# Optimization experiments

Hardware: AMD Instinct MI355X
Metric: run time of the kernel (lower is better)

Reference implementation:

```python
import jax, jax.numpy as jnp
from jax import lax
import numpy as np

B = 8; T = 64000
NFFT = 1024; HOP = 256
SC = 20; KS = 1024; PAD = 512
HEADS = 8; GH = 64; GO = 32
SPEC_DIM = 32 * (NFFT // 4) // 2   # 4096
NODE_DIM = SC + SPEC_DIM           # 4116
EPS = 1e-5
NEG_SLOPE = 0.2


def setup_inputs() -> dict:
    ks = jax.random.split(jax.random.key(0), 12)
    f32 = jnp.float32
    def rn(k, shp, s):
        return jax.random.normal(k, shp, dtype=f32) * s
    return {
        "x": jax.random.normal(ks[0], (B, 1, T), dtype=f32),
        "sinc_w": rn(ks[1], (SC, 1, KS), 0.03),
        "conv1_w": rn(ks[2], (32, 1, 3, 3), 0.1),
        "conv1_b": jnp.zeros((32,), f32),
        "bn1_g": jnp.ones((32,), f32),
        "bn1_b": jnp.zeros((32,), f32),
        "conv2_w": rn(ks[3], (32, 32, 3, 3), 0.06),
        "conv2_b": jnp.zeros((32,), f32),
        "bn2_g": jnp.ones((32,), f32),
        "bn2_b": jnp.zeros((32,), f32),
        "gat1_W": rn(ks[4], (NODE_DIM, HEADS * GH), 0.015),
        "gat1_asrc": rn(ks[5], (HEADS, GH), 0.1),
        "gat1_adst": rn(ks[6], (HEADS, GH), 0.1),
        "gat1_bias": jnp.zeros((HEADS * GH,), f32),
        "gat2_W": rn(ks[7], (HEADS * GH, GO), 0.04),
        "gat2_asrc": rn(ks[8], (1, GO), 0.1),
        "gat2_adst": rn(ks[9], (1, GO), 0.1),
        "gat2_bias": jnp.zeros((GO,), f32),
        "fc1_w": rn(ks[10], (GO, 128), 0.15),
        "fc1_b": jnp.zeros((128,), f32),
        "bnf_g": jnp.ones((128,), f32),
        "bnf_b": jnp.zeros((128,), f32),
        "fc2_w": rn(ks[11], (128, 2), 0.08),
        "fc2_b": jnp.zeros((2,), f32),
    }


def _bn2d_eval(z, g, b):
    # eval-mode BatchNorm2d with running_mean=0, running_var=1
    s = g / jnp.sqrt(1.0 + EPS)
    return z * s[None, :, None, None] + b[None, :, None, None]


def _conv2d(z, w, b):
    y = lax.conv_general_dilated(z, w, (1, 1), ((1, 1), (1, 1)),
                                 dimension_numbers=("NCHW", "OIHW", "NCHW"))
    return y + b[None, :, None, None]


def _gat_dense(hin, W, asrc, adst, bias, heads, fo, concat):
    # PyG GATConv on a fully-connected graph (add_self_loops=True default
    # => every node attends to all nodes including itself). Eval mode (no dropout).
    b, n, d = hin.shape
    h = jnp.einsum("bnd,dhf->bnhf", hin, W.reshape(d, heads, fo))
    s_src = jnp.einsum("bnhf,hf->bnh", h, asrc)   # alpha_j contribution
    s_dst = jnp.einsum("bnhf,hf->bnh", h, adst)   # alpha_i contribution
    e = jax.nn.leaky_relu(s_dst[:, :, None, :] + s_src[:, None, :, :], NEG_SLOPE)  # (b,i,j,h)
    a = jax.nn.softmax(e, axis=2)                 # softmax over sources j per dest i
    out = jnp.einsum("bijh,bjhf->bihf", a, h)
    out = out.reshape(b, n, heads * fo) if concat else out.mean(axis=2)
    return out + bias


def reference(x, sinc_w, conv1_w, conv1_b, bn1_g, bn1_b, conv2_w, conv2_b,
              bn2_g, bn2_b, gat1_W, gat1_asrc, gat1_adst, gat1_bias,
              gat2_W, gat2_asrc, gat2_adst, gat2_bias,
              fc1_w, fc1_b, bnf_g, bnf_b, fc2_w, fc2_b):
    b = x.shape[0]
    # --- sinc (band-pass) conv branch: conv1d k=1024, pad=512 ---
    sinc = lax.conv_general_dilated(x, sinc_w, (1,), ((PAD, PAD),),
                                    dimension_numbers=("NCH", "OIH", "NCH"))  # (b,20,T+1)
    Ls = (sinc.shape[-1] // 4) * 4
    sinc_feat = sinc[:, :, :Ls].reshape(b, SC, Ls // 4, 4).mean(-1)  # avg_pool1d(4)
    sinc_feat = jnp.transpose(sinc_feat, (0, 2, 1))                  # (b, Ls//4, 20)

    # --- STFT branch (torch.stft: center=True, reflect pad, rect window) ---
    xw = x[:, 0, :]
    xp = jnp.pad(xw, ((0, 0), (NFFT // 2, NFFT // 2)), mode="reflect")
    n_frames = 1 + T // HOP  # 251
    idx = np.arange(n_frames)[:, None] * HOP + np.arange(NFFT)
    frames = xp[:, idx]                                   # (b, 251, 1024)
    mag = jnp.abs(jnp.fft.rfft(frames, axis=-1))          # (b, 251, 513)
    logmag = jnp.log(mag + 1e-9)
    s = jnp.transpose(logmag, (0, 2, 1))[:, None]         # (b, 1, 513, 251)

    h = jax.nn.relu(_bn2d_eval(_conv2d(s, conv1_w, conv1_b), bn1_g, bn1_b))
    h = jax.nn.relu(_bn2d_eval(_conv2d(h, conv2_w, conv2_b), bn2_g, bn2_b))
    Fq = (h.shape[2] // 2) * 2
    Tt = (h.shape[3] // 2) * 2
    h = h[:, :, :Fq, :Tt].reshape(b, 32, Fq // 2, 2, Tt // 2, 2).max(axis=(3, 5))  # maxpool 2x2
    spec_feat = jnp.transpose(h, (0, 3, 1, 2)).reshape(b, -1, SPEC_DIM)  # (b, 250, 4096)

    n = min(sinc_feat.shape[1], spec_feat.shape[1])  # 250
    nodes = jnp.concatenate([sinc_feat[:, :n], spec_feat[:, :n]], axis=-1)  # (b,250,4116)

    g1 = jax.nn.relu(_gat_dense(nodes, gat1_W, gat1_asrc, gat1_adst, gat1_bias, HEADS, GH, True))
    g2 = _gat_dense(g1, gat2_W, gat2_asrc, gat2_adst, gat2_bias, 1, GO, False)
    emb = g2.mean(axis=1)  # (b, 32) graph-mean readout

    z = emb @ fc1_w + fc1_b
    z = jax.nn.relu(z * (bnf_g / jnp.sqrt(1.0 + EPS)) + bnf_b)  # eval BN1d
    out = z @ fc2_w + fc2_b
    return (out, emb)
```

## Files before the change

### kernel.cpp

```cpp
#include <hip/hip_runtime.h>
#include <hip/hip_bf16.h>
#include <math.h>

#define TB 8
#define TT 64000
#define NFRAMES 251
#define NROWS (TB*NFRAMES)
#define GROWS 2048
#define NBINS 513
#define NBPAD 576
#define NNODE 250
#define NODE_DIM 4116
#define KPAD 4128

typedef __attribute__((ext_vector_type(8))) short short8;
typedef __attribute__((ext_vector_type(4))) float floatx4;

static __device__ __forceinline__ unsigned short f2bf(float x) {
    __hip_bfloat16 h = __float2bfloat16(x);
    return *(unsigned short*)&h;
}
static __device__ __forceinline__ float bf2f(unsigned short u) {
    __hip_bfloat16 h = *(__hip_bfloat16*)&u;
    return __bfloat162float(h);
}

__global__ __launch_bounds__(256) void k_prep(
    const float* __restrict__ x, const float* __restrict__ sinc_w,
    const float* __restrict__ c2w, const float* __restrict__ g2bn,
    const float* __restrict__ W,
    unsigned short* __restrict__ fh, unsigned short* __restrict__ fl,
    unsigned short* __restrict__ bch, unsigned short* __restrict__ bcl,
    unsigned short* __restrict__ bsh, unsigned short* __restrict__ bsl,
    unsigned short* __restrict__ wbt, unsigned short* __restrict__ Bp,
    unsigned short* __restrict__ Wt, unsigned short* __restrict__ nodesb,
    unsigned short* __restrict__ h1t, unsigned short* __restrict__ h2t) {
    __shared__ unsigned short tile[64][65];
    int bi = blockIdx.x, tid = threadIdx.x;
    if (bi < 2048) {
        int idx = bi * 256 + tid;
        int row = idx >> 8, r = idx & 255;
        int b = row >> 8, j = row & 255;
        int u = j * 256 + r - 512;
        if (u < 0) u = -u;
        if (u >= TT) u = 2 * TT - 2 - u;
        float v = x[b * TT + u];
        unsigned short h = f2bf(v);
        fh[idx] = h;
        fl[idx] = f2bf(v - bf2f(h));
    } else if (bi < 2624) {
        int idx = (bi - 2048) * 256 + tid;
        int k = idx >> 8, r = idx & 255;
        float s = 0.f, c = 0.f;
        if (k < NBINS) {
            int mm = (k * r) & 1023;
            sincospif((float)mm * (1.0f / 512.0f), &s, &c);
        }
        unsigned short chv = f2bf(c), shv = f2bf(s);
        bch[idx] = chv; bcl[idx] = f2bf(c - bf2f(chv));
        bsh[idx] = shv; bsl[idx] = f2bf(s - bf2f(shv));
    } else if (bi < 3144) {
        int local = bi - 2624;
        int kt = local % 65, nt = local / 65;
        for (int idx = tid; idx < 4096; idx += 256) {
            int r = idx >> 6, c = idx & 63;
            int kp = kt * 64 + r;
            int k;
            if (kp < 20) k = kp;
            else if (kp < NODE_DIM) { int t = kp - 20; k = 20 + (t & 15) * 256 + (t >> 4); }
            else k = -1;
            float v = (k >= 0) ? W[k * 512 + nt * 64 + c] : 0.f;
            tile[r][c] = f2bf(v);
        }
        __syncthreads();
        for (int idx = tid; idx < 4096; idx += 256) {
            int nl = idx >> 6, kl = idx & 63;
            int k = kt * 64 + kl;
            if (k < KPAD)
                Wt[(size_t)(nt * 64 + nl) * KPAD + k] = tile[kl][nl];
        }
    } else if (bi < 3276) {
        int idx = (bi - 3144) * 256 + tid;
        if (idx < 32 * 1056) {
            int c = idx / 1056, m = idx - c * 1056;
            float s = 0.f;
            if (c < 20 && m < 1027) {
                #pragma unroll
                for (int d = 0; d < 4; d++) {
                    int k = m - d;
                    if (k >= 0 && k < 1024) s += sinc_w[c * 1024 + k];
                }
                s *= 0.25f;
            }
            wbt[idx] = f2bf(s);
        }
    } else if (bi < 3312) {
        int idx = (bi - 3276) * 256 + tid;
        if (idx < 9216) {
            int j = idx & 7, lane = (idx >> 3) & 63, ct = (idx >> 9) & 1, s = idx >> 10;
            int co = ct * 16 + (lane & 15);
            int ci = (lane >> 4) * 8 + j;
            float inv = rsqrtf(1.0f + 1e-5f);
            Bp[idx] = f2bf(c2w[co * 288 + ci * 9 + s] * (g2bn[co] * inv));
        }
    } else {
        int idx = (bi - 3312) * 256 + tid;
        if (idx < 24000) {
            int row = idx / 12, c = idx - row * 12;
            nodesb[(size_t)row * KPAD + 4116 + c] = 0;
        } else if (idx < 48576) {
            int t = idx - 24000; int r = t / 6, c = t - r * 6;
            h1t[(size_t)r * 256 + 250 + c] = 0;
        } else if (idx < 50112) {
            int t = idx - 48576; int r = t / 6, c = t - r * 6;
            h2t[(size_t)r * 256 + 250 + c] = 0;
        }
    }
}

__global__ __launch_bounds__(256) void k_sincm(const float* __restrict__ x,
                                               const unsigned short* __restrict__ wbt,
                                               unsigned short* __restrict__ nodesb) {
    __shared__ __align__(16) unsigned short xs[1312];
    int ut = blockIdx.x, b = blockIdx.y;
    int tid = threadIdx.x;
    int base = 256 * ut - 512;
    for (int i = tid; i < 1312; i += 256) {
        int g = base + i;
        float v = (g >= 0 && g < TT) ? x[b * TT + g] : 0.f;
        xs[i] = f2bf(v);
    }
    __syncthreads();
    int w = tid >> 6, lane = tid & 63;
    int q = lane >> 4, col = lane & 15;
    floatx4 acc[2];
    acc[0] = acc[1] = (floatx4){0.f, 0.f, 0.f, 0.f};
    for (int K0 = 0; K0 < 1056; K0 += 32) {
        int off = 4 * (w * 16 + col) + K0 + q * 8;
        unsigned long long lo = *(const unsigned long long*)&xs[off];
        unsigned long long hi = *(const unsigned long long*)&xs[off + 4];
        union { unsigned long long u64[2]; short8 s8; } cv;
        cv.u64[0] = lo; cv.u64[1] = hi;
        short8 af = cv.s8;
        #pragma unroll
        for (int ni = 0; ni < 2; ni++) {
            short8 bf = *(const short8*)(wbt + (size_t)(ni * 16 + col) * 1056 + K0 + q * 8);
            acc[ni] = __builtin_amdgcn_mfma_f32_16x16x32_bf16(af, bf, acc[ni], 0, 0, 0);
        }
    }
    #pragma unroll
    for (int ni = 0; ni < 2; ni++)
        #pragma unroll
        for (int rr = 0; rr < 4; rr++) {
            int u = ut * 64 + w * 16 + q * 4 + rr;
            int c = ni * 16 + col;
            if (u < NNODE && c < 20)
                nodesb[(size_t)(b * NNODE + u) * KPAD + c] = f2bf(acc[ni][rr]);
        }
}

__global__ __launch_bounds__(256) void k_dft_mfma(const unsigned short* __restrict__ fh,
                                                  const unsigned short* __restrict__ fl,
                                                  const unsigned short* __restrict__ ch,
                                                  const unsigned short* __restrict__ cl,
                                                  const unsigned short* __restrict__ sh,
                                                  const unsigned short* __restrict__ sl,
                                                  float* __restrict__ GRo,
                                                  float* __restrict__ GIo) {
    __shared__ __align__(16) unsigned short Ah[32 * 40];
    __shared__ __align__(16) unsigned short Al[32 * 40];
    __shared__ __align__(16) unsigned short Bch[64 * 40];
    __shared__ __align__(16) unsigned short Bcl[64 * 40];
    __shared__ __align__(16) unsigned short Bsh[64 * 40];
    __shared__ __align__(16) unsigned short Bsl[64 * 40];
    int tid = threadIdx.x;
    int N0 = blockIdx.x * 64, M0 = blockIdx.y * 32;
    int br = tid >> 2, bc = (tid & 3) * 8;
    size_t boff = (size_t)(N0 + br) * 256 + bc;
    int ar = (tid & 127) >> 2, ac = (tid & 3) * 8;
    size_t aoff = (size_t)(M0 + ar) * 256 + ac;
    bool loA = tid < 128;
    int w = tid >> 6, lane = tid & 63;
    int q = lane >> 4, col = lane & 15;
    int mb = (w >> 1) * 16, nb = (w & 1) * 32;
    floatx4 aR[2], aI[2];
    aR[0] = aR[1] = aI[0] = aI[1] = (floatx4){0.f, 0.f, 0.f, 0.f};

    for (int K0 = 0; K0 < 256; K0 += 32) {
        if (loA) *(short8*)&Ah[ar * 40 + ac] = *(const short8*)(fh + aoff + K0);
        else     *(short8*)&Al[ar * 40 + ac] = *(const short8*)(fl + aoff + K0);
        *(short8*)&Bch[br * 40 + bc] = *(const short8*)(ch + boff + K0);
        *(short8*)&Bcl[br * 40 + bc] = *(const short8*)(cl + boff + K0);
        *(short8*)&Bsh[br * 40 + bc] = *(const short8*)(sh + boff + K0);
        *(short8*)&Bsl[br * 40 + bc] = *(const short8*)(sl + boff + K0);
        __syncthreads();
        short8 ahv = *(const short8*)&Ah[(mb + col) * 40 + q * 8];
        short8 alv = *(const short8*)&Al[(mb + col) * 40 + q * 8];
        #pragma unroll
        for (int ni = 0; ni < 2; ni++) {
            short8 chv = *(const short8*)&Bch[(nb + ni * 16 + col) * 40 + q * 8];
            short8 clv = *(const short8*)&Bcl[(nb + ni * 16 + col) * 40 + q * 8];
            short8 shv = *(const short8*)&Bsh[(nb + ni * 16 + col) * 40 + q * 8];
            short8 slv = *(const short8*)&Bsl[(nb + ni * 16 + col) * 40 + q * 8];
            aR[ni] = __builtin_amdgcn_mfma_f32_16x16x32_bf16(ahv, chv, aR[ni], 0, 0, 0);
            aR[ni] = __builtin_amdgcn_mfma_f32_16x16x32_bf16(ahv, clv, aR[ni], 0, 0, 0);
            aR[ni] = __builtin_amdgcn_mfma_f32_16x16x32_bf16(alv, chv, aR[ni], 0, 0, 0);
            aI[ni] = __builtin_amdgcn_mfma_f32_16x16x32_bf16(ahv, shv, aI[ni], 0, 0, 0);
            aI[ni] = __builtin_amdgcn_mfma_f32_16x16x32_bf16(ahv, slv, aI[ni], 0, 0, 0);
            aI[ni] = __builtin_amdgcn_mfma_f32_16x16x32_bf16(alv, shv, aI[ni], 0, 0, 0);
        }
        __syncthreads();
    }
    #pragma unroll
    for (int ni = 0; ni < 2; ni++)
        #pragma unroll
        for (int rr = 0; rr < 4; rr++) {
            int m = M0 + mb + q * 4 + rr;
            int bin = N0 + nb + ni * 16 + col;
            GRo[(size_t)m * NBPAD + bin] = aR[ni][rr];
            GIo[(size_t)m * NBPAD + bin] = aI[ni][rr];
        }
}

__global__ __launch_bounds__(256) void k_dftcomb(const float* __restrict__ GR,
                                                 const float* __restrict__ GI,
                                                 float* __restrict__ S0) {
    int idx = blockIdx.x * 256 + threadIdx.x;
    if (idx >= NROWS * NBINS) return;
    int mg = idx / NBINS, bin = idx - mg * NBINS;
    int b = mg / NFRAMES, i = mg - b * NFRAMES;
    size_t base = ((size_t)(b * 256 + i)) * NBPAD + bin;
    float gr0 = GR[base], gr1 = GR[base + NBPAD], gr2 = GR[base + 2 * NBPAD], gr3 = GR[base + 3 * NBPAD];
    float gs0 = GI[base], gs1 = GI[base + NBPAD], gs2 = GI[base + 2 * NBPAD], gs3 = GI[base + 3 * NBPAD];
    float fre, fim;
    switch (bin & 3) {
        case 0: fre = gr0 + gr1 + gr2 + gr3; fim = gs0 + gs1 + gs2 + gs3; break;
        case 1: fre = gr0 - gs1 - gr2 + gs3; fim = gs0 + gr1 - gs2 - gr3; break;
        case 2: fre = gr0 - gr1 + gr2 - gr3; fim = gs0 - gs1 + gs2 - gs3; break;
        default: fre = gr0 + gs1 - gr2 - gs3; fim = gs0 - gr1 - gs2 + gr3; break;
    }
    S0[(b * NBINS + bin) * NFRAMES + i] = logf(sqrtf(fmaf(fre, fre, fim * fim)) + 1e-9f);
}

__global__ __launch_bounds__(256) void k_conv2f(const float* __restrict__ S0,
                                                const float* __restrict__ c1w,
                                                const float* __restrict__ c1b,
                                                const float* __restrict__ g1bn,
                                                const float* __restrict__ b1bn,
                                                const unsigned short* __restrict__ Bp,
                                                const float* __restrict__ c2b,
                                                const float* __restrict__ g2bn,
                                                const float* __restrict__ b2bn,
                                                unsigned short* __restrict__ nodesb) {
    __shared__ __align__(16) unsigned short o1s[18 * 18 * 32];
    __shared__ float S0s[20][20];
    __shared__ float w1s[288];
    __shared__ float b1s[32];
    __shared__ float b2s[32];
    int tid = threadIdx.x;
    int b = blockIdx.z;
    int F0 = blockIdx.y * 8;
    int T0 = blockIdx.x * 8;
    float inv = rsqrtf(1.0f + 1e-5f);
    if (tid < 32) {
        b1s[tid] = c1b[tid] * (g1bn[tid] * inv) + b1bn[tid];
        b2s[tid] = c2b[tid] * (g2bn[tid] * inv) + b2bn[tid];
    }
    for (int i = tid; i < 288; i += 256) w1s[i] = c1w[i] * (g1bn[i / 9] * inv);
    for (int i = tid; i < 400; i += 256) {
        int r = i / 20, c = i - r * 20;
        int rr = 2 * F0 - 2 + r, cc = 2 * T0 - 2 + c;
        float v = 0.f;
        if (rr >= 0 && rr < 513 && cc >= 0 && cc < 251)
            v = S0[((size_t)b * 513 + rr) * 251 + cc];
        S0s[r][c] = v;
    }
    __syncthreads();

    {
        int o = tid & 3;
        float wr[72];
        #pragma unroll
        for (int k = 0; k < 72; k++) wr[k] = w1s[o * 72 + k];
        float br[8];
        #pragma unroll
        for (int ci = 0; ci < 8; ci++) br[ci] = b1s[o * 8 + ci];
        for (int idx = tid; idx < 1296; idx += 256) {
            int r = idx / 72, rem = idx - r * 72;
            int t = rem >> 2;
            int r1 = 2 * F0 - 1 + r, t1 = 2 * T0 - 1 + t;
            bool valid = (r1 >= 0 && r1 < 513 && t1 >= 0 && t1 < 251);
            float sv[9];
            #pragma unroll
            for (int di = 0; di < 3; di++)
                #pragma unroll
                for (int dj = 0; dj < 3; dj++)
                    sv[di * 3 + dj] = S0s[r + di][t + dj];
            unsigned short ov[8];
            #pragma unroll
            for (int ci = 0; ci < 8; ci++) {
                float a = br[ci];
                #pragma unroll
                for (int k = 0; k < 9; k++) a = fmaf(sv[k], wr[ci * 9 + k], a);
                ov[ci] = valid ? f2bf(fmaxf(a, 0.f)) : (unsigned short)0;
            }
            *(short8*)&o1s[(size_t)(r * 18 + t) * 32 + o * 8] = *(const short8*)ov;
        }
    }
    __syncthreads();

    int lane = tid & 63, w = tid >> 6;
    int q = lane >> 4, col = lane & 15;
    floatx4 acc[4][2];
    #pragma unroll
    for (int rt = 0; rt < 4; rt++)
        #pragma unroll
        for (int ct = 0; ct < 2; ct++)
            acc[rt][ct] = (floatx4){0.f, 0.f, 0.f, 0.f};

    #pragma unroll
    for (int s = 0; s < 9; s++) {
        const int di = s / 3, dj = s % 3;
        short8 bf0 = *(const short8*)&Bp[(s * 2 + 0) * 512 + lane * 8];
        short8 bf1 = *(const short8*)&Bp[(s * 2 + 1) * 512 + lane * 8];
        #pragma unroll
        for (int rt = 0; rt < 4; rt++) {
            short8 af = *(const short8*)&o1s[((w * 4 + rt + di) * 18 + (col + dj)) * 32 + q * 8];
            acc[rt][0] = __builtin_amdgcn_mfma_f32_16x16x32_bf16(af, bf0, acc[rt][0], 0, 0, 0);
            acc[rt][1] = __builtin_amdgcn_mfma_f32_16x16x32_bf16(af, bf1, acc[rt][1], 0, 0, 0);
        }
    }
    __syncthreads();

    unsigned short* nb = o1s;
    #pragma unroll
    for (int ct = 0; ct < 2; ct++) {
        float bb = b2s[ct * 16 + col];
        #pragma unroll
        for (int fp2 = 0; fp2 < 2; fp2++)
            #pragma unroll
            for (int tc2 = 0; tc2 < 2; tc2++) {
                float m0 = fmaxf(
                    fmaxf(acc[2 * fp2][ct][2 * tc2], acc[2 * fp2][ct][2 * tc2 + 1]),
                    fmaxf(acc[2 * fp2 + 1][ct][2 * tc2], acc[2 * fp2 + 1][ct][2 * tc2 + 1]));
                float v = fmaxf(m0 + bb, 0.f);
                int nl = (2 * q + tc2) * 2 + ct;
                int fl = 2 * w + fp2;
                nb[nl * 136 + fl * 16 + col] = f2bf(v);
            }
    }
    __syncthreads();

    int nl = tid >> 4, part = tid & 15;
    int node_g = 2 * T0 + nl;
    if (node_g < NNODE) {
        unsigned short* dst = nodesb + (size_t)(b * NNODE + node_g) * KPAD + 20 + F0 * 16 + part * 8;
        *(short8*)(dst) = *(const short8*)&nb[nl * 136 + part * 8];
    }
}

__global__ __launch_bounds__(256) void k_gat1s(const unsigned short* __restrict__ A,
                                               const unsigned short* __restrict__ Bt,
                                               float* __restrict__ hpart) {
    __shared__ __align__(16) unsigned short As[64 * 40];
    __shared__ __align__(16) unsigned short Bs[64 * 40];
    int tid = threadIdx.x;
    int N0 = blockIdx.x * 64, M0 = blockIdx.y * 64;
    int kc = blockIdx.z;
    int ks = (kc == 0) ? 0 : (33 + 32 * (kc - 1));
    int ke = 33 + 32 * kc;
    if (kc == 0) ke = 33;
    int sr = tid >> 2, sc = (tid & 3) * 8;
    int w = tid >> 6, lane = tid & 63;
    int q = lane >> 4, col = lane & 15;
    int mb = (w >> 1) * 32, nb = (w & 1) * 32;
    floatx4 acc[2][2];
    acc[0][0] = acc[0][1] = acc[1][0] = acc[1][1] = (floatx4){0.f, 0.f, 0.f, 0.f};
    short8 z8 = {0, 0, 0, 0, 0, 0, 0, 0};
    int mA = M0 + sr;
    bool mv = mA < 2000;
    const unsigned short* pa = A + (size_t)mA * KPAD + sc;
    const unsigned short* pb = Bt + (size_t)(N0 + sr) * KPAD + sc;

    for (int kk = ks; kk < ke; kk++) {
        int K0 = kk * 32;
        short8 va = mv ? *(const short8*)(pa + K0) : z8;
        short8 vb = *(const short8*)(pb + K0);
        *(short8*)&As[sr * 40 + sc] = va;
        *(short8*)&Bs[sr * 40 + sc] = vb;
        __syncthreads();
        short8 a0 = *(const short8*)&As[(mb + col) * 40 + q * 8];
        short8 a1 = *(const short8*)&As[(mb + 16 + col) * 40 + q * 8];
        short8 b0 = *(const short8*)&Bs[(nb + col) * 40 + q * 8];
        short8 b1 = *(const short8*)&Bs[(nb + 16 + col) * 40 + q * 8];
        acc[0][0] = __builtin_amdgcn_mfma_f32_16x16x32_bf16(a0, b0, acc[0][0], 0, 0, 0);
        acc[0][1] = __builtin_amdgcn_mfma_f32_16x16x32_bf16(a0, b1, acc[0][1], 0, 0, 0);
        acc[1][0] = __builtin_amdgcn_mfma_f32_16x16x32_bf16(a1, b0, acc[1][0], 0, 0, 0);
        acc[1][1] = __builtin_amdgcn_mfma_f32_16x16x32_bf16(a1, b1, acc[1][1], 0, 0, 0);
        __syncthreads();
    }
    float* out = hpart + (size_t)kc * 1024000;
    #pragma unroll
    for (int mi = 0; mi < 2; mi++)
        #pragma unroll
        for (int ni = 0; ni < 2; ni++)
            #pragma unroll
            for (int rr = 0; rr < 4; rr++) {
                int m = M0 + mb + mi * 16 + q * 4 + rr;
                if (m < 2000)
                    out[m * 512 + N0 + nb + ni * 16 + col] = acc[mi][ni][rr];
            }
}

__global__ __launch_bounds__(256) void k_hred(const float* __restrict__ hpart,
                                              const float* __restrict__ asrc,
                                              const float* __restrict__ adst,
                                              unsigned short* __restrict__ h1t,
                                              float* __restrict__ ssrc,
                                              float* __restrict__ sdst) {
    int m = blockIdx.x;
    int tid = threadIdx.x;
    int n1 = tid, n2 = tid + 256;
    size_t base = (size_t)m * 512;
    float s1 = hpart[base + n1] + hpart[base + n1 + 1024000] +
               hpart[base + n1 + 2048000] + hpart[base + n1 + 3072000];
    float s2 = hpart[base + n2] + hpart[base + n2 + 1024000] +
               hpart[base + n2 + 2048000] + hpart[base + n2 + 3072000];
    int bb = m / NNODE, j = m - bb * NNODE;
    int hh1 = n1 >> 6, f1 = n1 & 63;
    int hh2 = n2 >> 6, f2 = n2 & 63;
    h1t[((size_t)((bb * 8 + hh1) * 64 + f1)) * 256 + j] = f2bf(s1);
    h1t[((size_t)((bb * 8 + hh2) * 64 + f2)) * 256 + j] = f2bf(s2);
    float ps1 = s1 * asrc[n1], pd1 = s1 * adst[n1];
    float ps2 = s2 * asrc[n2], pd2 = s2 * adst[n2];
    for (int off = 32; off > 0; off >>= 1) {
        ps1 += __shfl_down(ps1, off); pd1 += __shfl_down(pd1, off);
        ps2 += __shfl_down(ps2, off); pd2 += __shfl_down(pd2, off);
    }
    int lane = tid & 63, w = tid >> 6;
    if (lane == 0) {
        ssrc[m * 8 + w] = ps1;     sdst[m * 8 + w] = pd1;
        ssrc[m * 8 + 4 + w] = ps2; sdst[m * 8 + 4 + w] = pd2;
    }
}

__global__ __launch_bounds__(256) void k_attw(const float* __restrict__ ssrc,
                                              const float* __restrict__ sdst,
                                              unsigned short* __restrict__ Pn) {
    int bh = blockIdx.x;
    int b = bh >> 3, h = bh & 7;
    int tid = threadIdx.x;
    __shared__ float ss[NNODE];
    __shared__ float red[4];
    for (int j = tid; j < NNODE; j += 256) ss[j] = ssrc[(b * NNODE + j) * 8 + h];
    __syncthreads();
    float mv = (tid < NNODE) ? ss[tid] : -1e30f;
    for (int off = 32; off > 0; off >>= 1) mv = fmaxf(mv, __shfl_down(mv, off));
    if ((tid & 63) == 0) red[tid >> 6] = mv;
    __syncthreads();
    float smaxv = fmaxf(fmaxf(red[0], red[1]), fmaxf(red[2], red[3]));
    unsigned short* row = Pn + ((size_t)bh * 256 + tid) * 256;
    short8 z8 = {0, 0, 0, 0, 0, 0, 0, 0};
    if (tid >= NNODE) {
        #pragma unroll
        for (int j = 0; j < 256; j += 8) *(short8*)(row + j) = z8;
        return;
    }
    float d = sdst[(b * NNODE + tid) * 8 + h];
    float e0 = d + smaxv;
    float mx = e0 > 0.f ? e0 : 0.2f * e0;
    float den = 0.f;
    for (int j = 0; j < NNODE; j++) {
        float e = d + ss[j];
        e = e > 0.f ? e : 0.2f * e;
        den += __expf(e - mx);
    }
    float rden = 1.f / den;
    for (int j0 = 0; j0 < 256; j0 += 8) {
        unsigned short wv[8];
        #pragma unroll
        for (int jj = 0; jj < 8; jj++) {
            int j = j0 + jj;
            float wt = 0.f;
            if (j < NNODE) {
                float e = d + ss[j];
                e = e > 0.f ? e : 0.2f * e;
                wt = __expf(e - mx) * rden;
            }
            wv[jj] = f2bf(wt);
        }
        *(short8*)(row + j0) = *(const short8*)wv;
    }
}

__global__ __launch_bounds__(256) void k_attnv(const unsigned short* __restrict__ Pn,
                                               const unsigned short* __restrict__ h1t,
                                               const float* __restrict__ bias,
                                               float* __restrict__ g1) {
    int bh = blockIdx.x;
    int b = bh >> 3, h = bh & 7;
    int tid = threadIdx.x;
    int w = tid >> 6, lane = tid & 63;
    int q = lane >> 4, col = lane & 15;
    const unsigned short* Pb = Pn + (size_t)bh * 65536;
    const unsigned short* Hb = h1t + (size_t)bh * 16384;
    floatx4 acc[4][4];
    #pragma unroll
    for (int mi = 0; mi < 4; mi++)
        #pragma unroll
        for (int ni = 0; ni < 4; ni++)
            acc[mi][ni] = (floatx4){0.f, 0.f, 0.f, 0.f};
    for (int k0 = 0; k0 < 256; k0 += 32) {
        short8 af[4], bf[4];
        #pragma unroll
        for (int mi = 0; mi < 4; mi++)
            af[mi] = *(const short8*)(Pb + (size_t)((w * 4 + mi) * 16 + col) * 256 + k0 + q * 8);
        #pragma unroll
        for (int ni = 0; ni < 4; ni++)
            bf[ni] = *(const short8*)(Hb + (size_t)(ni * 16 + col) * 256 + k0 + q * 8);
        #pragma unroll
        for (int mi = 0; mi < 4; mi++)
            #pragma unroll
            for (int ni = 0; ni < 4; ni++)
                acc[mi][ni] = __builtin_amdgcn_mfma_f32_16x16x32_bf16(af[mi], bf[ni], acc[mi][ni], 0, 0, 0);
    }
    #pragma unroll
    for (int mi = 0; mi < 4; mi++)
        #pragma unroll
        for (int ni = 0; ni < 4; ni++)
            #pragma unroll
            for (int rr = 0; rr < 4; rr++) {
                int i = (w * 4 + mi) * 16 + q * 4 + rr;
                int f = ni * 16 + col;
                if (i < NNODE)
                    g1[(b * NNODE + i) * 512 + h * 64 + f] =
                        fmaxf(acc[mi][ni][rr] + bias[h * 64 + f], 0.f);
            }
}

__global__ __launch_bounds__(256) void k_h2(const float* __restrict__ g1,
                                            const float* __restrict__ W2,
                                            const float* __restrict__ a2src,
                                            const float* __restrict__ a2dst,
                                            unsigned short* __restrict__ h2t,
                                            float* __restrict__ s2src,
                                            float* __restrict__ s2dst) {
    int row = blockIdx.x * 4 + (threadIdx.x >> 6);
    if (row >= 2000) return;
    int lane = threadIdx.x & 63;
    int o = lane & 31, half = lane >> 5;
    const float* gr = &g1[row * 512 + half * 256];
    float acc = 0.f;
    for (int k = 0; k < 256; k++) acc = fmaf(gr[k], W2[(half * 256 + k) * 32 + o], acc);
    acc += __shfl_down(acc, 32);
    float ps = acc * a2src[o], pd = acc * a2dst[o];
    for (int off = 16; off > 0; off >>= 1) {
        ps += __shfl_down(ps, off, 32);
        pd += __shfl_down(pd, off, 32);
    }
    if (lane == 0) { s2src[row] = ps; s2dst[row] = pd; }
    if (lane < 32) {
        int b = row / NNODE, j = row - b * NNODE;
        h2t[((size_t)(b * 32 + o)) * 256 + j] = f2bf(acc);
    }
}

__global__ __launch_bounds__(256) void k_attw2(const float* __restrict__ s2src,
                                               const float* __restrict__ s2dst,
                                               unsigned short* __restrict__ P2n) {
    int b = blockIdx.x;
    int tid = threadIdx.x;
    __shared__ float ss[NNODE];
    __shared__ float red[4];
    for (int j = tid; j < NNODE; j += 256) ss[j] = s2src[b * NNODE + j];
    __syncthreads();
    float mv = (tid < NNODE) ? ss[tid] : -1e30f;
    for (int off = 32; off > 0; off >>= 1) mv = fmaxf(mv, __shfl_down(mv, off));
    if ((tid & 63) == 0) red[tid >> 6] = mv;
    __syncthreads();
    float smaxv = fmaxf(fmaxf(red[0], red[1]), fmaxf(red[2], red[3]));
    unsigned short* row = P2n + ((size_t)b * 256 + tid) * 256;
    short8 z8 = {0, 0, 0, 0, 0, 0, 0, 0};
    if (tid >= NNODE) {
        #pragma unroll
        for (int j = 0; j < 256; j += 8) *(short8*)(row + j) = z8;
        return;
    }
    float d = s2dst[b * NNODE + tid];
    float e0 = d + smaxv;
    float mx = e0 > 0.f ? e0 : 0.2f * e0;
    float den = 0.f;
    for (int j = 0; j < NNODE; j++) {
        float e = d + ss[j];
        e = e > 0.f ? e : 0.2f * e;
        den += __expf(e - mx);
    }
    float rden = 1.f / den;
    for (int j0 = 0; j0 < 256; j0 += 8) {
        unsigned short wv[8];
        #pragma unroll
        for (int jj = 0; jj < 8; jj++) {
            int j = j0 + jj;
            float wt = 0.f;
            if (j < NNODE) {
                float e = d + ss[j];
                e = e > 0.f ? e : 0.2f * e;
                wt = __expf(e - mx) * rden;
            }
            wv[jj] = f2bf(wt);
        }
        *(short8*)(row + j0) = *(const short8*)wv;
    }
}

__global__ __launch_bounds__(256) void k_attnv2(const unsigned short* __restrict__ P2n,
                                                const unsigned short* __restrict__ h2t,
                                                const float* __restrict__ bias2,
                                                float* __restrict__ g2) {
    int b = blockIdx.x;
    int tid = threadIdx.x;
    int w = tid >> 6, lane = tid & 63;
    int q = lane >> 4, col = lane & 15;
    const unsigned short* Pb = P2n + (size_t)b * 65536;
    const unsigned short* Hb = h2t + (size_t)b * 8192;
    floatx4 acc[4][2];
    #pragma unroll
    for (int mi = 0; mi < 4; mi++)
        #pragma unroll
        for (int ni = 0; ni < 2; ni++)
            acc[mi][ni] = (floatx4){0.f, 0.f, 0.f, 0.f};
    for (int k0 = 0; k0 < 256; k0 += 32) {
        short8 af[4], bf[2];
        #pragma unroll
        for (int mi = 0; mi < 4; mi++)
            af[mi] = *(const short8*)(Pb + (size_t)((w * 4 + mi) * 16 + col) * 256 + k0 + q * 8);
        #pragma unroll
        for (int ni = 0; ni < 2; ni++)
            bf[ni] = *(const short8*)(Hb + (size_t)(ni * 16 + col) * 256 + k0 + q * 8);
        #pragma unroll
        for (int mi = 0; mi < 4; mi++)
            #pragma unroll
            for (int ni = 0; ni < 2; ni++)
                acc[mi][ni] = __builtin_amdgcn_mfma_f32_16x16x32_bf16(af[mi], bf[ni], acc[mi][ni], 0, 0, 0);
    }
    #pragma unroll
    for (int mi = 0; mi < 4; mi++)
        #pragma unroll
        for (int ni = 0; ni < 2; ni++)
            #pragma unroll
            for (int rr = 0; rr < 4; rr++) {
                int i = (w * 4 + mi) * 16 + q * 4 + rr;
                int f = ni * 16 + col;
                if (i < NNODE)
                    g2[(b * NNODE + i) * 32 + f] = acc[mi][ni][rr] + bias2[f];
            }
}

__global__ __launch_bounds__(256) void k_fc(const float* __restrict__ g2,
                                            const float* __restrict__ fc1w,
                                            const float* __restrict__ fc1b,
                                            const float* __restrict__ bnfg,
                                            const float* __restrict__ bnfb,
                                            const float* __restrict__ fc2w,
                                            const float* __restrict__ fc2b,
                                            float* __restrict__ dout) {
    __shared__ float es[256];
    __shared__ float zs[1024];
    int tid = threadIdx.x;
    {
        int b = tid >> 5, f = tid & 31;
        float s = 0.f;
        #pragma unroll 5
        for (int i = 0; i < NNODE; i++) s += g2[((size_t)(b * NNODE + i)) * 32 + f];
        s *= (1.0f / 250.0f);
        es[tid] = s;
        dout[16 + tid] = s;
    }
    __syncthreads();
    float inv = rsqrtf(1.0f + 1e-5f);
    #pragma unroll
    for (int rep = 0; rep < 4; rep++) {
        int idx = tid + rep * 256;
        int b = idx >> 7, j = idx & 127;
        float a = fc1b[j];
        #pragma unroll
        for (int k = 0; k < 32; k++) a = fmaf(es[b * 32 + k], fc1w[k * 128 + j], a);
        a = a * (bnfg[j] * inv) + bnfb[j];
        zs[idx] = fmaxf(a, 0.f);
    }
    __syncthreads();
    if (tid < 16) {
        int b = tid >> 1, o = tid & 1;
        float a = fc2b[o];
        for (int k = 0; k < 128; k++) a = fmaf(zs[b * 128 + k], fc2w[k * 2 + o], a);
        dout[b * 2 + o] = a;
    }
}

extern "C" void kernel_launch(void* const* d_in, const int* in_sizes, int n_in,
                              void* d_out, int out_size, void* d_ws, size_t ws_size,
                              hipStream_t stream) {
    (void)in_sizes; (void)n_in; (void)out_size; (void)ws_size;
    const float* x       = (const float*)d_in[0];
    const float* sinc_w  = (const float*)d_in[1];
    const float* conv1_w = (const float*)d_in[2];
    const float* conv1_b = (const float*)d_in[3];
    const float* bn1_g   = (const float*)d_in[4];
    const float* bn1_b   = (const float*)d_in[5];
    const float* conv2_w = (const float*)d_in[6];
    const float* conv2_b = (const float*)d_in[7];
    const float* bn2_g   = (const float*)d_in[8];
    const float* bn2_b   = (const float*)d_in[9];
    const float* gat1_W  = (const float*)d_in[10];
    const float* gat1_as = (const float*)d_in[11];
    const float* gat1_ad = (const float*)d_in[12];
    const float* gat1_bi = (const float*)d_in[13];
    const float* gat2_W  = (const float*)d_in[14];
    const float* gat2_as = (const float*)d_in[15];
    const float* gat2_ad = (const float*)d_in[16];
    const float* gat2_bi = (const float*)d_in[17];
    const float* fc1_w   = (const float*)d_in[18];
    const float* fc1_b   = (const float*)d_in[19];
    const float* bnf_g   = (const float*)d_in[20];
    const float* bnf_b   = (const float*)d_in[21];
    const float* fc2_w   = (const float*)d_in[22];
    const float* fc2_b   = (const float*)d_in[23];
    float* dout = (float*)d_out;

    unsigned short* fh  = (unsigned short*)d_ws;
    unsigned short* fl  = fh + (size_t)GROWS * 256;
    unsigned short* bch = fl + (size_t)GROWS * 256;
    unsigned short* bcl = bch + (size_t)NBPAD * 256;
    unsigned short* bsh = bcl + (size_t)NBPAD * 256;
    unsigned short* bsl = bsh + (size_t)NBPAD * 256;
    float* GRb = (float*)(bsl + (size_t)NBPAD * 256);
    float* GIb = GRb + (size_t)GROWS * NBPAD;
    float* S0  = GIb + (size_t)GROWS * NBPAD;
    unsigned short* wbt = (unsigned short*)(S0 + 1030104);
    unsigned short* bpk = wbt + 32 * 1056;
    unsigned short* Wt  = bpk + 9216;
    unsigned short* nodesb = Wt + (size_t)512 * KPAD;
    unsigned short* Pn  = nodesb + (size_t)2000 * KPAD;
    unsigned short* h1t = Pn + (size_t)64 * 256 * 256;
    unsigned short* h2t = h1t + (size_t)64 * 64 * 256;
    unsigned short* P2n = h2t + (size_t)8 * 32 * 256;
    float* hpart = (float*)(P2n + (size_t)8 * 256 * 256);
    float* ssrc1 = hpart + 4 * 1024000;
    float* sdst1 = ssrc1 + 16000;
    float* g1    = sdst1 + 16000;
    float* s2src = g1 + 1024000;
    float* s2dst = s2src + 2000;
    float* g2    = s2dst + 2000;

    hipLaunchKernelGGL(k_prep, dim3(3508), dim3(256), 0, stream,
                       x, sinc_w, conv2_w, bn2_g, gat1_W,
                       fh, fl, bch, bcl, bsh, bsl, wbt, bpk, Wt, nodesb, h1t, h2t);
    hipLaunchKernelGGL(k_dft_mfma, dim3(9, 64), dim3(256), 0, stream,
                       fh, fl, bch, bcl, bsh, bsl, GRb, GIb);
    hipLaunchKernelGGL(k_dftcomb, dim3((NROWS * NBINS + 255) / 256), dim3(256), 0, stream,
                       GRb, GIb, S0);
    hipLaunchKernelGGL(k_sincm, dim3(4, 8), dim3(256), 0, stream, x, wbt, nodesb);
    hipLaunchKernelGGL(k_conv2f, dim3(16, 32, 8), dim3(256), 0, stream,
                       S0, conv1_w, conv1_b, bn1_g, bn1_b, bpk, conv2_b, bn2_g, bn2_b, nodesb);
    hipLaunchKernelGGL(k_gat1s, dim3(8, 32, 4), dim3(256), 0, stream, nodesb, Wt, hpart);
    hipLaunchKernelGGL(k_hred, dim3(2000), dim3(256), 0, stream,
                       hpart, gat1_as, gat1_ad, h1t, ssrc1, sdst1);
    hipLaunchKernelGGL(k_attw, dim3(64), dim3(256), 0, stream, ssrc1, sdst1, Pn);
    hipLaunchKernelGGL(k_attnv, dim3(64), dim3(256), 0, stream, Pn, h1t, gat1_bi, g1);
    hipLaunchKernelGGL(k_h2, dim3(500), dim3(256), 0, stream,
                       g1, gat2_W, gat2_as, gat2_ad, h2t, s2src, s2dst);
    hipLaunchKernelGGL(k_attw2, dim3(8), dim3(256), 0, stream, s2src, s2dst, P2n);
    hipLaunchKernelGGL(k_attnv2, dim3(8), dim3(256), 0, stream, P2n, h2t, gat2_bi, g2);
    hipLaunchKernelGGL(k_fc, dim3(1), dim3(256), 0, stream,
                       g2, fc1_w, fc1_b, bnf_g, bnf_b, fc2_w, fc2_b, dout);
}
```

Before: 343.3 us.

## Compute conv1 stage with MFMA using split-bf16 weights and inputs

Replaces the scalar FP32 first 3x3 convolution in the fused conv kernel with bf16 MFMA instructions. Inputs and weights are each split into high and low bf16 parts so the product stays close to FP32 accuracy. The K dimension is packed as hi*hi, lo*hi, hi*lo and the centre tap. A new prep section builds the packed weight matrix once, which removes the per-block weight staging and the scalar FMA loop. The cost is extra conversion work, lane-dependent fragment assembly and scattered 2-byte LDS stores for the output.

```diff
diff --git a/kernel.cpp b/kernel.cpp
--- a/kernel.cpp
+++ b/kernel.cpp
@@ -28,11 +28,13 @@
 __global__ __launch_bounds__(256) void k_prep(
     const float* __restrict__ x, const float* __restrict__ sinc_w,
     const float* __restrict__ c2w, const float* __restrict__ g2bn,
+    const float* __restrict__ c1w, const float* __restrict__ g1bn,
     const float* __restrict__ W,
     unsigned short* __restrict__ fh, unsigned short* __restrict__ fl,
     unsigned short* __restrict__ bch, unsigned short* __restrict__ bcl,
     unsigned short* __restrict__ bsh, unsigned short* __restrict__ bsl,
     unsigned short* __restrict__ wbt, unsigned short* __restrict__ Bp,
+    unsigned short* __restrict__ Bc1,
     unsigned short* __restrict__ Wt, unsigned short* __restrict__ nodesb,
     unsigned short* __restrict__ h1t, unsigned short* __restrict__ h2t) {
     __shared__ unsigned short tile[64][65];
@@ -103,7 +105,7 @@
             float inv = rsqrtf(1.0f + 1e-5f);
             Bp[idx] = f2bf(c2w[co * 288 + ci * 9 + s] * (g2bn[co] * inv));
         }
-    } else {
+    } else if (bi < 3508) {
         int idx = (bi - 3312) * 256 + tid;
         if (idx < 24000) {
             int row = idx / 12, c = idx - row * 12;
@@ -114,6 +116,26 @@
         } else if (idx < 50112) {
             int t = idx - 48576; int r = t / 6, c = t - r * 6;
             h2t[(size_t)r * 256 + 250 + c] = 0;
+        }
+    } else {
+        int idx = (bi - 3508) * 256 + tid;
+        if (idx < 1024) {
+            int ch = idx >> 5, k = idx & 31;
+            float inv = rsqrtf(1.0f + 1e-5f);
+            int t; int typ;
+            if (k < 8)       { t = k;      typ = 0; }
+            else if (k < 16) { t = k - 8;  typ = 0; }
+            else if (k < 24) { t = k - 16; typ = 1; }
+            else if (k == 24 || k == 25) { t = 8; typ = 0; }
+            else if (k == 26) { t = 8; typ = 1; }
+            else { t = 0; typ = 2; }
+            unsigned short outv = 0;
+            if (typ != 2) {
+                float wv = c1w[ch * 9 + t] * (g1bn[ch] * inv);
+                unsigned short whi = f2bf(wv);
+                outv = (typ == 0) ? whi : f2bf(wv - bf2f(whi));
+            }
+            Bc1[idx] = outv;
         }
     }
 }
@@ -243,7 +265,7 @@
 }
 
 __global__ __launch_bounds__(256) void k_conv2f(const float* __restrict__ S0,
-                                                const float* __restrict__ c1w,
+                                                const unsigned short* __restrict__ Bc1,
                                                 const float* __restrict__ c1b,
                                                 const float* __restrict__ g1bn,
                                                 const float* __restrict__ b1bn,
@@ -254,7 +276,6 @@
                                                 unsigned short* __restrict__ nodesb) {
     __shared__ __align__(16) unsigned short o1s[18 * 18 * 32];
     __shared__ float S0s[20][20];
-    __shared__ float w1s[288];
     __shared__ float b1s[32];
     __shared__ float b2s[32];
     int tid = threadIdx.x;
@@ -266,7 +287,6 @@
         b1s[tid] = c1b[tid] * (g1bn[tid] * inv) + b1bn[tid];
         b2s[tid] = c2b[tid] * (g2bn[tid] * inv) + b2bn[tid];
     }
-    for (int i = tid; i < 288; i += 256) w1s[i] = c1w[i] * (g1bn[i / 9] * inv);
     for (int i = tid; i < 400; i += 256) {
         int r = i / 20, c = i - r * 20;
         int rr = 2 * F0 - 2 + r, cc = 2 * T0 - 2 + c;
@@ -277,40 +297,61 @@
     }
     __syncthreads();
 
+    int lane = tid & 63, w = tid >> 6;
+    int q = lane >> 4, col = lane & 15;
+
     {
-        int o = tid & 3;
-        float wr[72];
-        #pragma unroll
-        for (int k = 0; k < 72; k++) wr[k] = w1s[o * 72 + k];
-        float br[8];
-        #pragma unroll
-        for (int ci = 0; ci < 8; ci++) br[ci] = b1s[o * 8 + ci];
-        for (int idx = tid; idx < 1296; idx += 256) {
-            int r = idx / 72, rem = idx - r * 72;
-            int t = rem >> 2;
-            int r1 = 2 * F0 - 1 + r, t1 = 2 * T0 - 1 + t;
-            bool valid = (r1 >= 0 && r1 < 513 && t1 >= 0 && t1 < 251);
-            float sv[9];
+        short8 bfr0 = *(const short8*)(Bc1 + (size_t)col * 32 + q * 8);
+        short8 bfr1 = *(const short8*)(Bc1 + (size_t)(16 + col) * 32 + q * 8);
+        for (int mt = w; mt < 21; mt += 4) {
+            int p = mt * 16 + col;
+            int pc = p < 324 ? p : 0;
+            int pr = (pc * 228) >> 12;
+            int pt = pc - pr * 18;
+            float tv[9];
             #pragma unroll
             for (int di = 0; di < 3; di++)
                 #pragma unroll
                 for (int dj = 0; dj < 3; dj++)
-                    sv[di * 3 + dj] = S0s[r + di][t + dj];
-            unsigned short ov[8];
+                    tv[di * 3 + dj] = S0s[pr + di][pt + dj];
+            unsigned short hu[9], lu[9];
             #pragma unroll
-            for (int ci = 0; ci < 8; ci++) {
-                float a = br[ci];
-                #pragma unroll
-                for (int k = 0; k < 9; k++) a = fmaf(sv[k], wr[ci * 9 + k], a);
-                ov[ci] = valid ? f2bf(fmaxf(a, 0.f)) : (unsigned short)0;
-            }
-            *(short8*)&o1s[(size_t)(r * 18 + t) * 32 + o * 8] = *(const short8*)ov;
-        }
-    }
-    __syncthreads();
-
-    int lane = tid & 63, w = tid >> 6;
-    int q = lane >> 4, col = lane & 15;
+            for (int i = 0; i < 9; i++) {
+                hu[i] = f2bf(tv[i]);
+                lu[i] = f2bf(tv[i] - bf2f(hu[i]));
+            }
+            short8 af;
+            if (q == 1) {
+                af[0] = lu[0]; af[1] = lu[1]; af[2] = lu[2]; af[3] = lu[3];
+                af[4] = lu[4]; af[5] = lu[5]; af[6] = lu[6]; af[7] = lu[7];
+            } else if (q == 3) {
+                af[0] = hu[8]; af[1] = lu[8]; af[2] = hu[8]; af[3] = 0;
+                af[4] = 0; af[5] = 0; af[6] = 0; af[7] = 0;
+            } else {
+                af[0] = hu[0]; af[1] = hu[1]; af[2] = hu[2]; af[3] = hu[3];
+                af[4] = hu[4]; af[5] = hu[5]; af[6] = hu[6]; af[7] = hu[7];
+            }
+            floatx4 c0 = (floatx4){0.f, 0.f, 0.f, 0.f};
+            floatx4 c1 = (floatx4){0.f, 0.f, 0.f, 0.f};
+            c0 = __builtin_amdgcn_mfma_f32_16x16x32_bf16(af, bfr0, c0, 0, 0, 0);
+            c1 = __builtin_amdgcn_mfma_f32_16x16x32_bf16(af, bfr1, c1, 0, 0, 0);
+            #pragma unroll
+            for (int rr2 = 0; rr2 < 4; rr2++) {
+                int pp = mt * 16 + q * 4 + rr2;
+                if (pp < 324) {
+                    int qr = (pp * 228) >> 12, qt = pp - qr * 18;
+                    int r1 = 2 * F0 - 1 + qr, t1 = 2 * T0 - 1 + qt;
+                    bool valid = (r1 >= 0 && r1 < 513 && t1 >= 0 && t1 < 251);
+                    float v0 = fmaxf(c0[rr2] + b1s[col], 0.f);
+                    float v1 = fmaxf(c1[rr2] + b1s[16 + col], 0.f);
+                    o1s[pp * 32 + col]      = valid ? f2bf(v0) : (unsigned short)0;
+                    o1s[pp * 32 + 16 + col] = valid ? f2bf(v1) : (unsigned short)0;
+                }
+            }
+        }
+    }
+    __syncthreads();
+
     floatx4 acc[4][2];
     #pragma unroll
     for (int rt = 0; rt < 4; rt++)
@@ -738,7 +779,8 @@
     float* S0  = GIb + (size_t)GROWS * NBPAD;
     unsigned short* wbt = (unsigned short*)(S0 + 1030104);
     unsigned short* bpk = wbt + 32 * 1056;
-    unsigned short* Wt  = bpk + 9216;
+    unsigned short* Bc1 = bpk + 9216;
+    unsigned short* Wt  = Bc1 + 1024;
     unsigned short* nodesb = Wt + (size_t)512 * KPAD;
     unsigned short* Pn  = nodesb + (size_t)2000 * KPAD;
     unsigned short* h1t = Pn + (size_t)64 * 256 * 256;
@@ -752,16 +794,16 @@
     float* s2dst = s2src + 2000;
     float* g2    = s2dst + 2000;
 
-    hipLaunchKernelGGL(k_prep, dim3(3508), dim3(256), 0, stream,
-                       x, sinc_w, conv2_w, bn2_g, gat1_W,
-                       fh, fl, bch, bcl, bsh, bsl, wbt, bpk, Wt, nodesb, h1t, h2t);
+    hipLaunchKernelGGL(k_prep, dim3(3512), dim3(256), 0, stream,
+                       x, sinc_w, conv2_w, bn2_g, conv1_w, bn1_g, gat1_W,
+                       fh, fl, bch, bcl, bsh, bsl, wbt, bpk, Bc1, Wt, nodesb, h1t, h2t);
     hipLaunchKernelGGL(k_dft_mfma, dim3(9, 64), dim3(256), 0, stream,
                        fh, fl, bch, bcl, bsh, bsl, GRb, GIb);
     hipLaunchKernelGGL(k_dftcomb, dim3((NROWS * NBINS + 255) / 256), dim3(256), 0, stream,
                        GRb, GIb, S0);
     hipLaunchKernelGGL(k_sincm, dim3(4, 8), dim3(256), 0, stream, x, wbt, nodesb);
     hipLaunchKernelGGL(k_conv2f, dim3(16, 32, 8), dim3(256), 0, stream,
-                       S0, conv1_w, conv1_b, bn1_g, bn1_b, bpk, conv2_b, bn2_g, bn2_b, nodesb);
+                       S0, Bc1, conv1_b, bn1_g, bn1_b, bpk, conv2_b, bn2_g, bn2_b, nodesb);
     hipLaunchKernelGGL(k_gat1s, dim3(8, 32, 4), dim3(256), 0, stream, nodesb, Wt, hpart);
     hipLaunchKernelGGL(k_hred, dim3(2000), dim3(256), 0, stream,
                        hpart, gat1_as, gat1_ad, h1t, ssrc1, sdst1);
```

Result: slower. 351.6 us (+2.4%).
